# Kernel optimization log

Measured on AMD Instinct MI355X. Metric: run time of the kernel, lower is better.

The kernel has to match this reference:

```python
import jax, jax.numpy as jnp
import numpy as np

N_NODES = 10000
N_EDGES = 640000
NODE_DIM = 128
EDGE_DIM = 32
OUT_DIM = 128


def setup_inputs() -> dict:
    key = jax.random.key(0)
    k_h, k_e, k_ef, k_w1, k_w2 = jax.random.split(key, 5)
    h = jax.random.normal(k_h, (N_NODES, NODE_DIM), dtype=jnp.float32)
    edge_index = jax.random.randint(k_e, (2, N_EDGES), 0, N_NODES, dtype=jnp.int64)
    edge_features = jax.random.normal(k_ef, (N_EDGES, EDGE_DIM), dtype=jnp.float32)
    in_dim = 2 * NODE_DIM + EDGE_DIM
    # Kaiming-ish init scale for realism
    W1 = jax.random.normal(k_w1, (in_dim, OUT_DIM), dtype=jnp.float32) / np.sqrt(in_dim)
    b1 = jnp.zeros((OUT_DIM,), dtype=jnp.float32)
    W2 = jax.random.normal(k_w2, (OUT_DIM, OUT_DIM), dtype=jnp.float32) / np.sqrt(OUT_DIM)
    b2 = jnp.zeros((OUT_DIM,), dtype=jnp.float32)
    return {"h": h, "edge_index": edge_index, "edge_features": edge_features,
            "n": N_NODES, "W1": W1, "b1": b1, "W2": W2, "b2": b2}


def reference(h, edge_index, edge_features, n, W1, b1, W2, b2):
    rows, cols = edge_index[0], edge_index[1]
    # gather source/target node features + edge features -> [E, 2*node_dim+edge_dim]
    msg_input = jnp.concatenate([h[rows], h[cols], edge_features], axis=-1)
    hidden = jax.nn.relu(msg_input @ W1 + b1)   # [E, out_dim]
    messages = hidden @ W2 + b2                 # [E, out_dim]
    # scatter-add messages onto destination rows -> [n, out_dim]
    out = jax.ops.segment_sum(messages, rows, num_segments=n)
    return out
```

## Files before the change

### kernel.cpp

```cpp
#include <hip/hip_runtime.h>
#include <hip/hip_bf16.h>


typedef __attribute__((ext_vector_type(8))) short bf16x8;
typedef __attribute__((ext_vector_type(4))) float f32x4;

#define ND 128
#define ED 32
#define NL1 2048

__device__ __forceinline__ short f2bf(float x) {
  unsigned int u = __float_as_uint(x);
  unsigned int r = (u + 0x7FFFu + ((u >> 16) & 1u)) >> 16;
  return (short)r;
}

__device__ __forceinline__ float bf2f(short s) {
  return __uint_as_float(((unsigned int)(unsigned short)s) << 16);
}

__device__ __forceinline__ f32x4 bf8lo(bf16x8 v) {
  f32x4 r;
  #pragma unroll
  for (int j = 0; j < 4; ++j) r[j] = bf2f(v[j]);
  return r;
}
__device__ __forceinline__ f32x4 bf8hi(bf16x8 v) {
  f32x4 r;
  #pragma unroll
  for (int j = 0; j < 4; ++j) r[j] = bf2f(v[4 + j]);
  return r;
}

__device__ __forceinline__ int swz(int c) {
  int ct = c >> 4, cc = c & 15;
  return (ct >> 2) * 64 + (cc >> 2) * 16 + (ct & 3) * 4 + (cc & 3);
}

__global__ __launch_bounds__(256) void prep_hist_kernel(
    const float* __restrict__ W1, const float* __restrict__ W2,
    const void* __restrict__ ei, int* __restrict__ counts,
    int* __restrict__ rank, unsigned int* __restrict__ rc,
    short* __restrict__ w12t, short* __restrict__ w1eA, short* __restrict__ w2t,
    int E) {
  int b = blockIdx.x;
  if (b < 128) {
    int t = b * 256 + threadIdx.x;
    if (t < 256 * 128) {
      int np = t >> 7, k = t & 127;
      float v = (np < 128) ? W1[k * 128 + np] : W1[(128 + k) * 128 + (np - 128)];
      w12t[t] = f2bf(v);
    }
    if (t < 128 * 128) {
      int n = t >> 7, k = t & 127;
      w2t[t] = f2bf(W2[k * 128 + n]);
    }
    if (t < 8 * 64 * 8) {
      int ct = t >> 9, lane = (t >> 3) & 63, j = t & 7;
      int li = lane & 15, lg = lane >> 4;
      w1eA[t] = f2bf(W1[(256 + lg * 8 + j) * 128 + ct * 16 + li]);
    }
  } else {
    int e = (b - 128) * 256 + threadIdx.x;
    if (e < E) {
      const unsigned int* u = (const unsigned int*)ei;
      int is64 = 1;
      #pragma unroll
      for (int i = 0; i < 16; ++i)
        if (u[2 * i + 1] != 0u) is64 = 0;
      int r, c;
      if (is64) {
        r = (int)((const long long*)ei)[e];
        c = (int)((const long long*)ei)[(long long)E + e];
      } else {
        r = ((const int*)ei)[e];
        c = ((const int*)ei)[E + e];
      }
      rank[e] = atomicAdd(&counts[r], 1);
      rc[e] = ((unsigned int)r << 16) | (unsigned int)c;
    }
  }
}

__global__ __launch_bounds__(1024) void scan_kernel(const int* __restrict__ counts,
                                                    int* __restrict__ row_ptr, int n) {
  __shared__ int wtot[16];
  int tid = threadIdx.x;
  int lane = tid & 63, w = tid >> 6;
  int base_i = tid * 16;
  int c[16];
  int tot = 0;
  #pragma unroll
  for (int j = 0; j < 16; ++j) {
    int i = base_i + j;
    c[j] = (i < n) ? counts[i] : 0;
    tot += c[j];
  }
  int x = tot;
  #pragma unroll
  for (int d = 1; d < 64; d <<= 1) {
    int t = __shfl_up(x, d);
    if (lane >= d) x += t;
  }
  if (lane == 63) wtot[w] = x;
  __syncthreads();
  if (w == 0) {
    int y = (lane < 16) ? wtot[lane] : 0;
    #pragma unroll
    for (int d = 1; d < 16; d <<= 1) {
      int t = __shfl_up(y, d);
      if (lane >= d) y += t;
    }
    if (lane < 16) wtot[lane] = y;
  }
  __syncthreads();
  int waveoff = (w == 0) ? 0 : wtot[w - 1];
  int run = waveoff + x - tot;
  if (tid == 0) row_ptr[0] = 0;
  #pragma unroll
  for (int j = 0; j < 16; ++j) {
    int i = base_i + j;
    if (i < n) {
      run += c[j];
      row_ptr[i + 1] = run;
    }
  }
}

__global__ __launch_bounds__(256, 4) void scatter_sg_kernel(
    const float* __restrict__ ef, const int* __restrict__ row_ptr,
    const int* __restrict__ rank, const unsigned int* __restrict__ rc,
    const float* __restrict__ h, const short* __restrict__ w12t,
    const float* __restrict__ b1, short* __restrict__ efb,
    int* __restrict__ ccol, float* __restrict__ s2, short* __restrict__ g2,
    int N, int E) {
  int b = blockIdx.x;
  int SGB = (N + 63) >> 6;
  if (b < SGB) {
    int lane = threadIdx.x & 63, w = threadIdx.x >> 6;
    int li = lane & 15, lg = lane >> 4;
    int base = b * 64 + w * 16;
    int rowm = base + li;
    if (rowm >= N) rowm = N - 1;
    float breg[8];
    #pragma unroll
    for (int nt = 0; nt < 8; ++nt) breg[nt] = b1[nt * 16 + li];
    f32x4 acc[16];
    #pragma unroll
    for (int nt = 0; nt < 16; ++nt) acc[nt] = (f32x4){0.f, 0.f, 0.f, 0.f};
    #pragma unroll
    for (int kc = 0; kc < 4; ++kc) {
      f32x4 f0 = *(const f32x4*)(h + (size_t)rowm * ND + kc * 32 + lg * 8);
      f32x4 f1 = *(const f32x4*)(h + (size_t)rowm * ND + kc * 32 + lg * 8 + 4);
      bf16x8 a;
      #pragma unroll
      for (int j = 0; j < 4; ++j) { a[j] = f2bf(f0[j]); a[4 + j] = f2bf(f1[j]); }
      #pragma unroll
      for (int nt = 0; nt < 16; ++nt) {
        bf16x8 bb = *(const bf16x8*)(w12t + (nt * 16 + li) * 128 + kc * 32 + lg * 8);
        acc[nt] = __builtin_amdgcn_mfma_f32_16x16x32_bf16(a, bb, acc[nt], 0, 0, 0);
      }
    }
    #pragma unroll
    for (int nt = 0; nt < 16; ++nt)
      #pragma unroll
      for (int r = 0; r < 4; ++r) {
        int row = base + lg * 4 + r;
        if (row < N) {
          if (nt < 8) {
            s2[(size_t)row * 128 + swz(nt * 16 + li)] = acc[nt][r] + breg[nt];
          } else {
            g2[(size_t)row * 128 + swz((nt - 8) * 16 + li)] = f2bf(acc[nt][r]);
          }
        }
      }
  } else {
    int gt = (b - SGB) * 256 + threadIdx.x;
    int e = gt >> 2, part = gt & 3;
    if (e < E) {
      unsigned int p = rc[e];
      int r = (int)(p >> 16), c = (int)(p & 0xffffu);
      int pos = row_ptr[r] + rank[e];
      f32x4 a0 = *(const f32x4*)(ef + (size_t)e * ED + part * 8);
      f32x4 a1 = *(const f32x4*)(ef + (size_t)e * ED + part * 8 + 4);
      bf16x8 ob;
      #pragma unroll
      for (int j = 0; j < 4; ++j) { ob[j] = f2bf(a0[j]); ob[4 + j] = f2bf(a1[j]); }
      *(bf16x8*)(efb + (size_t)pos * ED + part * 8) = ob;
      if (part == 0) ccol[pos] = c;
    }
  }
}

__global__ __launch_bounds__(128, 4) void layer1_kernel(
    const float* __restrict__ s2, const short* __restrict__ g2,
    const short* __restrict__ efb, const int* __restrict__ ccol,
    const short* __restrict__ w1eA, const int* __restrict__ row_ptr,
    float* __restrict__ hsum, int N) {
  int lane = threadIdx.x & 63;
  int w = threadIdx.x >> 6;
  int li = lane & 15, lg = lane >> 4;

  bf16x8 wa[4];
  #pragma unroll
  for (int nt = 0; nt < 4; ++nt)
    wa[nt] = *(const bf16x8*)(w1eA + ((w * 4 + nt) * 64 + lane) * 8);

  for (int node = blockIdx.x; node < N; node += NL1) {
    int rp = row_ptr[node], rpe = row_ptr[node + 1];
    int deg = rpe - rp;

    if (deg == 0) {
      if (li == 0) {
        #pragma unroll
        for (int nt = 0; nt < 4; ++nt)
          *(f32x4*)(hsum + (size_t)node * 128 + w * 64 + nt * 16 + lg * 4) =
              (f32x4){0.f, 0.f, 0.f, 0.f};
      }
      continue;
    }

    f32x4 sreg[4];
    #pragma unroll
    for (int nt = 0; nt < 4; ++nt)
      sreg[nt] = *(const f32x4*)(s2 + (size_t)node * 128 + w * 64 + lg * 16 + nt * 4);
    f32x4 psum[4];
    #pragma unroll
    for (int nt = 0; nt < 4; ++nt) psum[nt] = (f32x4){0.f, 0.f, 0.f, 0.f};

    int ntiles = (deg + 15) >> 4;
    int last = rpe - 1;
    auto ldpos = [&](int t) {
      int p = rp + t * 16 + li;
      return p > last ? last : p;
    };

    int pA = ldpos(0), pB = ldpos(1);
    int cA = ccol[pA], cB = ccol[pB];
    bf16x8 eA = *(const bf16x8*)(efb + (size_t)pA * ED + lg * 8);
    bf16x8 eB = *(const bf16x8*)(efb + (size_t)pB * ED + lg * 8);
    const short* gpA = g2 + (size_t)cA * 128 + w * 64 + lg * 16;
    bf16x8 gA0 = *(const bf16x8*)gpA;
    bf16x8 gA1 = *(const bf16x8*)(gpA + 8);

    for (int t = 0; t < ntiles; ++t) {
      const short* gpB = g2 + (size_t)cB * 128 + w * 64 + lg * 16;
      bf16x8 gB0 = *(const bf16x8*)gpB;
      bf16x8 gB1 = *(const bf16x8*)(gpB + 8);
      int pC = ldpos(t + 2);
      int cC = ccol[pC];
      bf16x8 eC = *(const bf16x8*)(efb + (size_t)pC * ED + lg * 8);
      f32x4 a0 = __builtin_amdgcn_mfma_f32_16x16x32_bf16(wa[0], eA, (f32x4){0.f,0.f,0.f,0.f}, 0, 0, 0);
      f32x4 a1 = __builtin_amdgcn_mfma_f32_16x16x32_bf16(wa[1], eA, (f32x4){0.f,0.f,0.f,0.f}, 0, 0, 0);
      f32x4 a2 = __builtin_amdgcn_mfma_f32_16x16x32_bf16(wa[2], eA, (f32x4){0.f,0.f,0.f,0.f}, 0, 0, 0);
      f32x4 a3 = __builtin_amdgcn_mfma_f32_16x16x32_bf16(wa[3], eA, (f32x4){0.f,0.f,0.f,0.f}, 0, 0, 0);
      if ((t * 16 + li) < deg) {
        f32x4 v0 = a0 + sreg[0] + bf8lo(gA0);
        f32x4 v1 = a1 + sreg[1] + bf8hi(gA0);
        f32x4 v2 = a2 + sreg[2] + bf8lo(gA1);
        f32x4 v3 = a3 + sreg[3] + bf8hi(gA1);
        #pragma unroll
        for (int r = 0; r < 4; ++r) {
          psum[0][r] += (v0[r] > 0.f ? v0[r] : 0.f);
          psum[1][r] += (v1[r] > 0.f ? v1[r] : 0.f);
          psum[2][r] += (v2[r] > 0.f ? v2[r] : 0.f);
          psum[3][r] += (v3[r] > 0.f ? v3[r] : 0.f);
        }
      }
      cB = cC; eA = eB; eB = eC;
      gA0 = gB0; gA1 = gB1;
    }

    #pragma unroll
    for (int nt = 0; nt < 4; ++nt)
      #pragma unroll
      for (int r = 0; r < 4; ++r) {
        float v = psum[nt][r];
        v += __shfl_xor(v, 1);
        v += __shfl_xor(v, 2);
        v += __shfl_xor(v, 4);
        v += __shfl_xor(v, 8);
        psum[nt][r] = v;
      }
    if (li == 0) {
      #pragma unroll
      for (int nt = 0; nt < 4; ++nt)
        *(f32x4*)(hsum + (size_t)node * 128 + w * 64 + nt * 16 + lg * 4) = psum[nt];
    }
  }
}

__global__ __launch_bounds__(256) void out_kernel(const float* __restrict__ hsum,
                                                  const short* __restrict__ w2t,
                                                  const float* __restrict__ b2,
                                                  const int* __restrict__ row_ptr,
                                                  float* __restrict__ out, int N) {
  int lane = threadIdx.x & 63, w = threadIdx.x >> 6;
  int li = lane & 15, lg = lane >> 4;
  int base = blockIdx.x * 64 + w * 16;
  int rowm = base + li;
  if (rowm >= N) rowm = N - 1;
  float breg[8];
  #pragma unroll
  for (int nt = 0; nt < 8; ++nt) breg[nt] = b2[nt * 16 + li];
  f32x4 acc[8];
  #pragma unroll
  for (int nt = 0; nt < 8; ++nt) acc[nt] = (f32x4){0.f, 0.f, 0.f, 0.f};
  #pragma unroll
  for (int kc = 0; kc < 4; ++kc) {
    f32x4 f0 = *(const f32x4*)(hsum + (size_t)rowm * 128 + kc * 32 + lg * 8);
    f32x4 f1 = *(const f32x4*)(hsum + (size_t)rowm * 128 + kc * 32 + lg * 8 + 4);
    bf16x8 a;
    #pragma unroll
    for (int j = 0; j < 4; ++j) { a[j] = f2bf(f0[j]); a[4 + j] = f2bf(f1[j]); }
    #pragma unroll
    for (int nt = 0; nt < 8; ++nt) {
      bf16x8 bb = *(const bf16x8*)(w2t + (nt * 16 + li) * 128 + kc * 32 + lg * 8);
      acc[nt] = __builtin_amdgcn_mfma_f32_16x16x32_bf16(a, bb, acc[nt], 0, 0, 0);
    }
  }
  #pragma unroll
  for (int r = 0; r < 4; ++r) {
    int row = base + lg * 4 + r;
    if (row < N) {
      float dg = (float)(row_ptr[row + 1] - row_ptr[row]);
      #pragma unroll
      for (int nt = 0; nt < 8; ++nt)
        out[(size_t)row * 128 + nt * 16 + li] = acc[nt][r] + dg * breg[nt];
    }
  }
}

extern "C" void kernel_launch(void* const* d_in, const int* in_sizes, int n_in,
                              void* d_out, int out_size, void* d_ws, size_t ws_size,
                              hipStream_t stream) {
  const float* h  = (const float*)d_in[0];
  const void*  ei = d_in[1];
  const float* ef = (const float*)d_in[2];
  const float* W1 = (const float*)d_in[4];
  const float* b1 = (const float*)d_in[5];
  const float* W2 = (const float*)d_in[6];
  const float* b2 = (const float*)d_in[7];
  float* out = (float*)d_out;
  int N = in_sizes[0] / ND;
  int E = in_sizes[2] / ED;

  char* ws = (char*)d_ws;
  size_t off = 0;
  auto alloc = [&](size_t bytes) {
    size_t o = off;
    off = (off + bytes + 255) & ~(size_t)255;
    return o;
  };
  int*          counts  = (int*)(ws + alloc((size_t)N * 4));
  int*          row_ptr = (int*)(ws + alloc((size_t)(N + 1) * 4));
  int*          rank    = (int*)(ws + alloc((size_t)E * 4));
  unsigned int* rc      = (unsigned int*)(ws + alloc((size_t)E * 4));
  short*        w12t    = (short*)(ws + alloc(256 * 128 * 2));
  short*        w1eA    = (short*)(ws + alloc(8 * 64 * 8 * 2));
  short*        w2t     = (short*)(ws + alloc(128 * 128 * 2));
  float*        s2      = (float*)(ws + alloc((size_t)N * 128 * 4));
  short*        g2      = (short*)(ws + alloc((size_t)N * 128 * 2));
  float*        hsumb   = (float*)(ws + alloc((size_t)N * 128 * 4));
  short*        efb     = (short*)(ws + alloc((size_t)E * ED * 2));
  int*          ccol    = (int*)(ws + alloc((size_t)E * 4));

  int SGB = (N + 63) >> 6;
  int SCB = (4 * E + 255) >> 8;

  hipMemsetAsync(counts, 0, (size_t)N * 4, stream);
  prep_hist_kernel<<<128 + (E + 255) / 256, 256, 0, stream>>>(
      W1, W2, ei, counts, rank, rc, w12t, w1eA, w2t, E);
  scan_kernel<<<1, 1024, 0, stream>>>(counts, row_ptr, N);
  scatter_sg_kernel<<<SGB + SCB, 256, 0, stream>>>(
      ef, row_ptr, rank, rc, h, w12t, b1, efb, ccol, s2, g2, N, E);
  layer1_kernel<<<NL1, 128, 0, stream>>>(s2, g2, efb, ccol, w1eA, row_ptr, hsumb, N);
  out_kernel<<<(N + 63) / 64, 256, 0, stream>>>(hsumb, w2t, b2, row_ptr, out, N);
}
```

Measured before the change: 133.8 us.

## Process all 128 output columns per wave in layer1, one wave per block

The layer1 kernel now uses a single 64-lane wave per block that computes all eight 16-column tiles. Before, two waves split the columns and each gathered the same edge features and column indices. The block count doubles so the number of waves stays the same. This removes the duplicated per-edge index and edge-feature loads across waves, at the cost of more registers per wave (8 weight fragments, accumulators and four gathered vectors), which may lower occupancy.

```diff
diff --git a/kernel.cpp b/kernel.cpp
--- a/kernel.cpp
+++ b/kernel.cpp
@@ -7,7 +7,7 @@
 
 #define ND 128
 #define ED 32
-#define NL1 2048
+#define NL1 4096
 
 __device__ __forceinline__ short f2bf(float x) {
   unsigned int u = __float_as_uint(x);
@@ -192,19 +192,18 @@
   }
 }
 
-__global__ __launch_bounds__(128, 4) void layer1_kernel(
+__global__ __launch_bounds__(64) void layer1_kernel(
     const float* __restrict__ s2, const short* __restrict__ g2,
     const short* __restrict__ efb, const int* __restrict__ ccol,
     const short* __restrict__ w1eA, const int* __restrict__ row_ptr,
     float* __restrict__ hsum, int N) {
   int lane = threadIdx.x & 63;
-  int w = threadIdx.x >> 6;
   int li = lane & 15, lg = lane >> 4;
 
-  bf16x8 wa[4];
-  #pragma unroll
-  for (int nt = 0; nt < 4; ++nt)
-    wa[nt] = *(const bf16x8*)(w1eA + ((w * 4 + nt) * 64 + lane) * 8);
+  bf16x8 wa[8];
+  #pragma unroll
+  for (int ct = 0; ct < 8; ++ct)
+    wa[ct] = *(const bf16x8*)(w1eA + (ct * 64 + lane) * 8);
 
   for (int node = blockIdx.x; node < N; node += NL1) {
     int rp = row_ptr[node], rpe = row_ptr[node + 1];
@@ -213,20 +212,21 @@
     if (deg == 0) {
       if (li == 0) {
         #pragma unroll
-        for (int nt = 0; nt < 4; ++nt)
-          *(f32x4*)(hsum + (size_t)node * 128 + w * 64 + nt * 16 + lg * 4) =
+        for (int ct = 0; ct < 8; ++ct)
+          *(f32x4*)(hsum + (size_t)node * 128 + ct * 16 + lg * 4) =
               (f32x4){0.f, 0.f, 0.f, 0.f};
       }
       continue;
     }
 
-    f32x4 sreg[4];
-    #pragma unroll
-    for (int nt = 0; nt < 4; ++nt)
-      sreg[nt] = *(const f32x4*)(s2 + (size_t)node * 128 + w * 64 + lg * 16 + nt * 4);
-    f32x4 psum[4];
-    #pragma unroll
-    for (int nt = 0; nt < 4; ++nt) psum[nt] = (f32x4){0.f, 0.f, 0.f, 0.f};
+    f32x4 sreg[8];
+    #pragma unroll
+    for (int ct = 0; ct < 8; ++ct)
+      sreg[ct] = *(const f32x4*)(s2 + (size_t)node * 128 +
+                                 (ct >> 2) * 64 + lg * 16 + (ct & 3) * 4);
+    f32x4 psum[8];
+    #pragma unroll
+    for (int ct = 0; ct < 8; ++ct) psum[ct] = (f32x4){0.f, 0.f, 0.f, 0.f};
 
     int ntiles = (deg + 15) >> 4;
     int last = rpe - 1;
@@ -239,53 +239,56 @@
     int cA = ccol[pA], cB = ccol[pB];
     bf16x8 eA = *(const bf16x8*)(efb + (size_t)pA * ED + lg * 8);
     bf16x8 eB = *(const bf16x8*)(efb + (size_t)pB * ED + lg * 8);
-    const short* gpA = g2 + (size_t)cA * 128 + w * 64 + lg * 16;
-    bf16x8 gA0 = *(const bf16x8*)gpA;
-    bf16x8 gA1 = *(const bf16x8*)(gpA + 8);
+    const short* gpA = g2 + (size_t)cA * 128;
+    bf16x8 gA0 = *(const bf16x8*)(gpA + lg * 16);
+    bf16x8 gA1 = *(const bf16x8*)(gpA + lg * 16 + 8);
+    bf16x8 gA2 = *(const bf16x8*)(gpA + 64 + lg * 16);
+    bf16x8 gA3 = *(const bf16x8*)(gpA + 64 + lg * 16 + 8);
 
     for (int t = 0; t < ntiles; ++t) {
-      const short* gpB = g2 + (size_t)cB * 128 + w * 64 + lg * 16;
-      bf16x8 gB0 = *(const bf16x8*)gpB;
-      bf16x8 gB1 = *(const bf16x8*)(gpB + 8);
+      const short* gpB = g2 + (size_t)cB * 128;
+      bf16x8 gB0 = *(const bf16x8*)(gpB + lg * 16);
+      bf16x8 gB1 = *(const bf16x8*)(gpB + lg * 16 + 8);
+      bf16x8 gB2 = *(const bf16x8*)(gpB + 64 + lg * 16);
+      bf16x8 gB3 = *(const bf16x8*)(gpB + 64 + lg * 16 + 8);
       int pC = ldpos(t + 2);
       int cC = ccol[pC];
       bf16x8 eC = *(const bf16x8*)(efb + (size_t)pC * ED + lg * 8);
-      f32x4 a0 = __builtin_amdgcn_mfma_f32_16x16x32_bf16(wa[0], eA, (f32x4){0.f,0.f,0.f,0.f}, 0, 0, 0);
-      f32x4 a1 = __builtin_amdgcn_mfma_f32_16x16x32_bf16(wa[1], eA, (f32x4){0.f,0.f,0.f,0.f}, 0, 0, 0);
-      f32x4 a2 = __builtin_amdgcn_mfma_f32_16x16x32_bf16(wa[2], eA, (f32x4){0.f,0.f,0.f,0.f}, 0, 0, 0);
-      f32x4 a3 = __builtin_amdgcn_mfma_f32_16x16x32_bf16(wa[3], eA, (f32x4){0.f,0.f,0.f,0.f}, 0, 0, 0);
+      f32x4 acc[8];
+      #pragma unroll
+      for (int ct = 0; ct < 8; ++ct)
+        acc[ct] = __builtin_amdgcn_mfma_f32_16x16x32_bf16(
+            wa[ct], eA, (f32x4){0.f, 0.f, 0.f, 0.f}, 0, 0, 0);
       if ((t * 16 + li) < deg) {
-        f32x4 v0 = a0 + sreg[0] + bf8lo(gA0);
-        f32x4 v1 = a1 + sreg[1] + bf8hi(gA0);
-        f32x4 v2 = a2 + sreg[2] + bf8lo(gA1);
-        f32x4 v3 = a3 + sreg[3] + bf8hi(gA1);
         #pragma unroll
-        for (int r = 0; r < 4; ++r) {
-          psum[0][r] += (v0[r] > 0.f ? v0[r] : 0.f);
-          psum[1][r] += (v1[r] > 0.f ? v1[r] : 0.f);
-          psum[2][r] += (v2[r] > 0.f ? v2[r] : 0.f);
-          psum[3][r] += (v3[r] > 0.f ? v3[r] : 0.f);
+        for (int ct = 0; ct < 8; ++ct) {
+          bf16x8 gr = (ct < 4) ? ((ct & 2) ? gA1 : gA0) : ((ct & 2) ? gA3 : gA2);
+          f32x4 gv = (ct & 1) ? bf8hi(gr) : bf8lo(gr);
+          f32x4 v = acc[ct] + sreg[ct] + gv;
+          #pragma unroll
+          for (int r = 0; r < 4; ++r)
+            psum[ct][r] += (v[r] > 0.f ? v[r] : 0.f);
         }
       }
       cB = cC; eA = eB; eB = eC;
-      gA0 = gB0; gA1 = gB1;
-    }
-
-    #pragma unroll
-    for (int nt = 0; nt < 4; ++nt)
+      gA0 = gB0; gA1 = gB1; gA2 = gB2; gA3 = gB3;
+    }
+
+    #pragma unroll
+    for (int ct = 0; ct < 8; ++ct)
       #pragma unroll
       for (int r = 0; r < 4; ++r) {
-        float v = psum[nt][r];
+        float v = psum[ct][r];
         v += __shfl_xor(v, 1);
         v += __shfl_xor(v, 2);
         v += __shfl_xor(v, 4);
         v += __shfl_xor(v, 8);
-        psum[nt][r] = v;
+        psum[ct][r] = v;
       }
     if (li == 0) {
       #pragma unroll
-      for (int nt = 0; nt < 4; ++nt)
-        *(f32x4*)(hsum + (size_t)node * 128 + w * 64 + nt * 16 + lg * 4) = psum[nt];
+      for (int ct = 0; ct < 8; ++ct)
+        *(f32x4*)(hsum + (size_t)node * 128 + ct * 16 + lg * 4) = psum[ct];
     }
   }
 }
@@ -374,6 +377,6 @@
   scan_kernel<<<1, 1024, 0, stream>>>(counts, row_ptr, N);
   scatter_sg_kernel<<<SGB + SCB, 256, 0, stream>>>(
       ef, row_ptr, rank, rc, h, w12t, b1, efb, ccol, s2, g2, N, E);
-  layer1_kernel<<<NL1, 128, 0, stream>>>(s2, g2, efb, ccol, w1eA, row_ptr, hsumb, N);
+  layer1_kernel<<<NL1, 64, 0, stream>>>(s2, g2, efb, ccol, w1eA, row_ptr, hsumb, N);
   out_kernel<<<(N + 63) / 64, 256, 0, stream>>>(hsumb, w2t, b2, row_ptr, out, N);
 }
```

Result: no change. 134.8 us (+0.8%).
